# Kernel tuning notes

Measured on AMD Instinct MI355X. Metric: run time of the kernel, lower is better.

The kernel has to match this reference:

```python
import jax, jax.numpy as jnp
import numpy as np

M, N, K = 1024, 11008, 4096


def _unpack_i2u(Bp):
    """Unpack 2-bit unsigned weights per decode_i2u_to_i8s interleave.

    Bp: [N, K//4] int8 storage. Within each group of 4 bytes (16 elements),
    output element at position 4*i + j = (byte_j >> (2*i)) & 3.
    Returns [N, K] int8 with values in {0,1,2,3}.
    """
    Bu = jax.lax.bitcast_convert_type(Bp, jnp.uint8)  # [N, K//4]
    n, kc = Bu.shape
    Bg = Bu.reshape(n, kc // 4, 1, 4)                 # [N, G, 1, j]
    shifts = (jnp.arange(4, dtype=jnp.uint8) * jnp.uint8(2)).reshape(1, 1, 4, 1)
    vals = (Bg >> shifts) & jnp.uint8(3)              # [N, G, i, j]
    return vals.reshape(n, kc * 4).astype(jnp.int8)   # [N, K]


def setup_inputs() -> dict:
    key = jax.random.key(0)
    k1, k2 = jax.random.split(key)
    A = jax.random.randint(k1, (M, K), -128, 128, dtype=jnp.int8)
    B = jax.random.randint(k2, (N, K // 4), -128, 128, dtype=jnp.int8)
    return {"A": A, "B": B}


def reference(A, B):
    W = _unpack_i2u(B)  # [N, K] int8
    C = jax.lax.dot_general(
        A, W,
        dimension_numbers=(((1,), (1,)), ((), ())),
        preferred_element_type=jnp.int32,
    )  # [M, N] int32
    return C
```

## Files before the change

### kernel.cpp

```cpp
#include <hip/hip_runtime.h>
#include <stdint.h>


#define MM 1024
#define NN 11008
#define KK 4096
#define KSTEPS 64
#define MTILES 8
#define NTILES 86
#define NBLOCKS (MTILES * NTILES)
#define STRIDE_A ((size_t)MTILES * 8192)
#define STRIDE_B ((size_t)NTILES * 2048)

using i32x4  = __attribute__((ext_vector_type(4))) int;
using i32x16 = __attribute__((ext_vector_type(16))) int;

__device__ __forceinline__ int pack4(i32x4 v) {
    return (int)(((uint32_t)v[0] & 0xFFu) | (((uint32_t)v[1] & 0xFFu) << 8)
               | (((uint32_t)v[2] & 0xFFu) << 16) | (((uint32_t)v[3] & 0xFFu) << 24));
}

__global__ __launch_bounds__(256) void prep_AB(const int* __restrict__ Asrc,
                                               const int* __restrict__ Bsrc,
                                               uint8_t* __restrict__ A2,
                                               uint8_t* __restrict__ B3) {
    if (blockIdx.x < 1024) {
        const int g = blockIdx.x * 256 + threadIdx.x;
        const int kstep = g >> 12;
        const int rem   = g & 4095;
        const int mtile = rem >> 9;
        const int c     = rem & 511;
        const int row32 = (c >> 7) & 3, kk2 = (c >> 6) & 1;
        const int lane  = c & 63;
        const int row   = mtile * 128 + row32 * 32 + (lane & 31);
        const int kbyte = kstep * 64 + kk2 * 32 + (lane >> 5) * 16;
        const i32x4* s4 = (const i32x4*)(Asrc + (size_t)row * KK + kbyte);
        i32x4 o;
#pragma unroll
        for (int q = 0; q < 4; ++q) o[q] = pack4(s4[q]);
        *(i32x4*)(A2 + (size_t)g * 16) = o;
    } else {
        const int t = (blockIdx.x - 1024) * 256 + threadIdx.x;
        const int n = t >> 6, kstep = t & 63;
        const int ntile = n >> 7, wc = (n >> 6) & 1, ni = (n >> 5) & 1, l31 = n & 31;
        const i32x4* s4 = (const i32x4*)(Bsrc + (size_t)n * (KK / 4) + kstep * 16);
        int w[4];
#pragma unroll
        for (int j = 0; j < 4; ++j) w[j] = pack4(s4[j]);
        uint8_t* base = B3 + ((size_t)kstep * NTILES + ntile) * 2048 + wc * 1024;
        *(int2*)(base + l31 * 16 + ni * 8)        = make_int2(w[0], w[2]);
        *(int2*)(base + (l31 + 32) * 16 + ni * 8) = make_int2(w[1], w[3]);
    }
}

#define GLOAD_LDS16(g, l) __builtin_amdgcn_global_load_lds(                    \
        (const __attribute__((address_space(1))) uint32_t*)(g),                \
        (__attribute__((address_space(3))) uint32_t*)(l), 16, 0, 0)

#define MFMA_I8 __builtin_amdgcn_mfma_i32_32x32x32_i8

#define STAGE(KS, SLOT) do {                                                   \
    const uint8_t* at_ = gA + (size_t)(KS) * STRIDE_A;                         \
    GLOAD_LDS16(at_,        &As[SLOT][wave * 1024]);                           \
    GLOAD_LDS16(at_ + 4096, &As[SLOT][4096 + wave * 1024]);                    \
} while (0)

#define BLOAD(BI, KS) bb[BI] = *(const i32x4*)(gB + (size_t)(KS) * STRIDE_B)

#define COMP(SLOT, BI) do {                                                    \
    _Pragma("unroll")                                                          \
    for (int kk2_ = 0; kk2_ < 2; ++kk2_) {                                     \
        i32x4 a0_ = *(const i32x4*)(&As[SLOT][(wr * 2 + 0) * 2048 + kk2_ * 1024 + lane * 16]); \
        i32x4 a1_ = *(const i32x4*)(&As[SLOT][(wr * 2 + 1) * 2048 + kk2_ * 1024 + lane * 16]); \
        const uint32_t q0_ = (uint32_t)bb[BI][0 * 2 + kk2_];                   \
        const uint32_t q1_ = (uint32_t)bb[BI][1 * 2 + kk2_];                   \
        i32x4 b0_, b1_;                                                        \
        _Pragma("unroll")                                                      \
        for (int i_ = 0; i_ < 4; ++i_) {                                       \
            b0_[i_] = (int)((q0_ >> (2 * i_)) & 0x03030303u);                  \
            b1_[i_] = (int)((q1_ >> (2 * i_)) & 0x03030303u);                  \
        }                                                                      \
        acc[0][0] = MFMA_I8(a0_, b0_, acc[0][0], 0, 0, 0);                     \
        acc[0][1] = MFMA_I8(a0_, b1_, acc[0][1], 0, 0, 0);                     \
        acc[1][0] = MFMA_I8(a1_, b0_, acc[1][0], 0, 0, 0);                     \
        acc[1][1] = MFMA_I8(a1_, b1_, acc[1][1], 0, 0, 0);                     \
    }                                                                          \
} while (0)

#define ITER(T, SLOT, BCUR, BNXT, NW, DOSTAGE, DOB) do {                       \
    asm volatile("s_waitcnt vmcnt(" #NW ")" ::: "memory");                     \
    __builtin_amdgcn_s_barrier();                                              \
    asm volatile("" ::: "memory");                                             \
    __builtin_amdgcn_sched_barrier(0);                                         \
    if (DOSTAGE) STAGE((T) + 5, ((SLOT) + 5) % 6);                             \
    if (DOB) BLOAD(BNXT, (T) + 2);                                             \
    COMP(SLOT, BCUR);                                                          \
} while (0)

__global__ __launch_bounds__(256, 3) void bitnet_gemm(const uint8_t* __restrict__ A2,
                                                      const uint8_t* __restrict__ B3,
                                                      int* __restrict__ C) {
    const int tid  = threadIdx.x;
    const int lane = tid & 63, wave = tid >> 6;
    const int wr   = wave >> 1, wc = wave & 1;
    const int l31  = lane & 31, h = lane >> 5;

    const int bid = blockIdx.x;
    const int l   = (bid & 7) * (NBLOCKS / 8) + (bid >> 3);
    const int bm  = l & 7;
    const int bn  = l >> 3;

    __shared__ __align__(16) uint8_t As[6][8192];

    const uint8_t* gA = A2 + (size_t)bm * 8192 + tid * 16;
    const uint8_t* gB = B3 + (size_t)bn * 2048 + wc * 1024 + lane * 16;

    i32x16 acc[2][2] = {};
    i32x4 bb[3];

    STAGE(0, 0); STAGE(1, 1); STAGE(2, 2); STAGE(3, 3); STAGE(4, 4);
    BLOAD(0, 0); BLOAD(1, 1);

#pragma unroll 1
    for (int t = 0; t < 54; t += 6) {
        ITER(t + 0, 0, 0, 2, 10, true, true);
        ITER(t + 1, 1, 1, 0, 10, true, true);
        ITER(t + 2, 2, 2, 1, 10, true, true);
        ITER(t + 3, 3, 0, 2, 10, true, true);
        ITER(t + 4, 4, 1, 0, 10, true, true);
        ITER(t + 5, 5, 2, 1, 10, true, true);
    }
    ITER(54, 0, 0, 2, 10, true,  true);
    ITER(55, 1, 1, 0, 10, true,  true);
    ITER(56, 2, 2, 1, 10, true,  true);
    ITER(57, 3, 0, 2, 10, true,  true);
    ITER(58, 4, 1, 0, 10, true,  true);
    ITER(59, 5, 2, 1, 10, false, true);
    ITER(60, 0, 0, 2, 10, false, true);
    ITER(61, 1, 1, 0, 8,  false, true);
    ITER(62, 2, 2, 1, 6,  false, false);
    ITER(63, 3, 0, 2, 4,  false, false);

    const int brow = bm * 128, bcol = bn * 128;
#pragma unroll
    for (int mi = 0; mi < 2; ++mi)
#pragma unroll
        for (int ni = 0; ni < 2; ++ni) {
            const int colg = bcol + wc * 64 + ni * 32 + l31;
#pragma unroll
            for (int r = 0; r < 16; ++r) {
                const int rowin = (r & 3) + 8 * (r >> 2) + 4 * h;
                const int rowg  = brow + wr * 64 + mi * 32 + rowin;
                C[(size_t)rowg * NN + colg] = acc[mi][ni][r];
            }
        }
}

extern "C" void kernel_launch(void* const* d_in, const int* in_sizes, int n_in,
                              void* d_out, int out_size, void* d_ws, size_t ws_size,
                              hipStream_t stream) {
    const int* A32 = (const int*)d_in[0];
    const int* B32 = (const int*)d_in[1];
    int* C = (int*)d_out;

    uint8_t* A2 = (uint8_t*)d_ws;
    uint8_t* B3 = A2 + (size_t)MM * KK;

    prep_AB<<<dim3(1024 + 2752), dim3(256), 0, stream>>>(A32, B32, A2, B3);
    bitnet_gemm<<<dim3(NBLOCKS), dim3(256), 0, stream>>>(A2, B3, C);
}
```

Before: 64.43 us.

## Process two k-steps per barrier with triple-buffered 16KB LDS stages

Restructures the main loop so each iteration consumes two 64-wide k-steps. Each stage is a 16KB LDS buffer, triple-buffered instead of the previous six 8KB slots, and B register prefetch is reduced to one double-k-step ahead. This halves the number of barriers and waitcnt points per K loop and issues larger batches of async loads. The cost is a shallower prefetch depth in k-steps, which may expose more global memory latency.

```diff
diff --git a/kernel.cpp b/kernel.cpp
--- a/kernel.cpp
+++ b/kernel.cpp
@@ -5,7 +5,6 @@
 #define MM 1024
 #define NN 11008
 #define KK 4096
-#define KSTEPS 64
 #define MTILES 8
 #define NTILES 86
 #define NBLOCKS (MTILES * NTILES)
@@ -42,12 +41,12 @@
     } else {
         const int t = (blockIdx.x - 1024) * 256 + threadIdx.x;
         const int n = t >> 6, kstep = t & 63;
-        const int ntile = n >> 7, wc = (n >> 6) & 1, ni = (n >> 5) & 1, l31 = n & 31;
+        const int ntile = n >> 7, hf = (n >> 6) & 1, ni = (n >> 5) & 1, l31 = n & 31;
         const i32x4* s4 = (const i32x4*)(Bsrc + (size_t)n * (KK / 4) + kstep * 16);
         int w[4];
 #pragma unroll
         for (int j = 0; j < 4; ++j) w[j] = pack4(s4[j]);
-        uint8_t* base = B3 + ((size_t)kstep * NTILES + ntile) * 2048 + wc * 1024;
+        uint8_t* base = B3 + ((size_t)kstep * NTILES + ntile) * 2048 + hf * 1024;
         *(int2*)(base + l31 * 16 + ni * 8)        = make_int2(w[0], w[2]);
         *(int2*)(base + (l31 + 32) * 16 + ni * 8) = make_int2(w[1], w[3]);
     }
@@ -59,42 +58,57 @@
 
 #define MFMA_I8 __builtin_amdgcn_mfma_i32_32x32x32_i8
 
-#define STAGE(KS, SLOT) do {                                                   \
-    const uint8_t* at_ = gA + (size_t)(KS) * STRIDE_A;                         \
-    GLOAD_LDS16(at_,        &As[SLOT][wave * 1024]);                           \
-    GLOAD_LDS16(at_ + 4096, &As[SLOT][4096 + wave * 1024]);                    \
+#define STAGE2(SL, T2) do {                                                    \
+    const uint8_t* s0_ = gA + (size_t)(2 * (T2)) * STRIDE_A;                   \
+    const uint8_t* s1_ = s0_ + STRIDE_A;                                       \
+    uint8_t* l_ = &As[SL][0];                                                  \
+    GLOAD_LDS16(s0_,        l_ + wave * 1024);                                 \
+    GLOAD_LDS16(s0_ + 4096, l_ + 4096 + wave * 1024);                          \
+    GLOAD_LDS16(s1_,        l_ + 8192 + wave * 1024);                          \
+    GLOAD_LDS16(s1_ + 4096, l_ + 12288 + wave * 1024);                         \
 } while (0)
 
-#define BLOAD(BI, KS) bb[BI] = *(const i32x4*)(gB + (size_t)(KS) * STRIDE_B)
+#define BLOAD2(BI, T2) do {                                                    \
+    bb0[BI] = *(const i32x4*)(gB + (size_t)(2 * (T2)) * STRIDE_B);             \
+    bb1[BI] = *(const i32x4*)(gB + (size_t)(2 * (T2) + 1) * STRIDE_B);         \
+} while (0)
 
-#define COMP(SLOT, BI) do {                                                    \
+#define COMP2(SL, BI) do {                                                     \
     _Pragma("unroll")                                                          \
-    for (int kk2_ = 0; kk2_ < 2; ++kk2_) {                                     \
-        i32x4 a0_ = *(const i32x4*)(&As[SLOT][(wr * 2 + 0) * 2048 + kk2_ * 1024 + lane * 16]); \
-        i32x4 a1_ = *(const i32x4*)(&As[SLOT][(wr * 2 + 1) * 2048 + kk2_ * 1024 + lane * 16]); \
-        const uint32_t q0_ = (uint32_t)bb[BI][0 * 2 + kk2_];                   \
-        const uint32_t q1_ = (uint32_t)bb[BI][1 * 2 + kk2_];                   \
-        i32x4 b0_, b1_;                                                        \
+    for (int sub_ = 0; sub_ < 2; ++sub_) {                                     \
+        const uint8_t* ab_ = &As[SL][sub_ * 8192];                             \
+        const i32x4 bv_ = sub_ ? bb1[BI] : bb0[BI];                            \
+        i32x4 aA0_ = *(const i32x4*)(ab_ + (wr * 2 + 0) * 2048 + lane * 16);   \
+        i32x4 aA1_ = *(const i32x4*)(ab_ + (wr * 2 + 0) * 2048 + 1024 + lane * 16); \
+        i32x4 aB0_ = *(const i32x4*)(ab_ + (wr * 2 + 1) * 2048 + lane * 16);   \
+        i32x4 aB1_ = *(const i32x4*)(ab_ + (wr * 2 + 1) * 2048 + 1024 + lane * 16); \
         _Pragma("unroll")                                                      \
-        for (int i_ = 0; i_ < 4; ++i_) {                                       \
-            b0_[i_] = (int)((q0_ >> (2 * i_)) & 0x03030303u);                  \
-            b1_[i_] = (int)((q1_ >> (2 * i_)) & 0x03030303u);                  \
+        for (int kk2_ = 0; kk2_ < 2; ++kk2_) {                                 \
+            const uint32_t q0_ = (uint32_t)bv_[kk2_];                          \
+            const uint32_t q1_ = (uint32_t)bv_[2 + kk2_];                      \
+            i32x4 b0_, b1_;                                                    \
+            _Pragma("unroll")                                                  \
+            for (int i_ = 0; i_ < 4; ++i_) {                                   \
+                b0_[i_] = (int)((q0_ >> (2 * i_)) & 0x03030303u);              \
+                b1_[i_] = (int)((q1_ >> (2 * i_)) & 0x03030303u);              \
+            }                                                                  \
+            const i32x4 am0_ = kk2_ ? aA1_ : aA0_;                             \
+            const i32x4 am1_ = kk2_ ? aB1_ : aB0_;                             \
+            acc[0][0] = MFMA_I8(am0_, b0_, acc[0][0], 0, 0, 0);                \
+            acc[0][1] = MFMA_I8(am0_, b1_, acc[0][1], 0, 0, 0);                \
+            acc[1][0] = MFMA_I8(am1_, b0_, acc[1][0], 0, 0, 0);                \
+            acc[1][1] = MFMA_I8(am1_, b1_, acc[1][1], 0, 0, 0);                \
         }                                                                      \
-        acc[0][0] = MFMA_I8(a0_, b0_, acc[0][0], 0, 0, 0);                     \
-        acc[0][1] = MFMA_I8(a0_, b1_, acc[0][1], 0, 0, 0);                     \
-        acc[1][0] = MFMA_I8(a1_, b0_, acc[1][0], 0, 0, 0);                     \
-        acc[1][1] = MFMA_I8(a1_, b1_, acc[1][1], 0, 0, 0);                     \
     }                                                                          \
 } while (0)
 
-#define ITER(T, SLOT, BCUR, BNXT, NW, DOSTAGE, DOB) do {                       \
+#define ITER2(T, SL, SLN, BI, BN, NW, DS, DB) do {                             \
     asm volatile("s_waitcnt vmcnt(" #NW ")" ::: "memory");                     \
     __builtin_amdgcn_s_barrier();                                              \
-    asm volatile("" ::: "memory");                                             \
     __builtin_amdgcn_sched_barrier(0);                                         \
-    if (DOSTAGE) STAGE((T) + 5, ((SLOT) + 5) % 6);                             \
-    if (DOB) BLOAD(BNXT, (T) + 2);                                             \
-    COMP(SLOT, BCUR);                                                          \
+    if (DB) BLOAD2(BN, (T) + 1);                                               \
+    if (DS) STAGE2(SLN, (T) + 2);                                              \
+    COMP2(SL, BI);                                                             \
 } while (0)
 
 __global__ __launch_bounds__(256, 3) void bitnet_gemm(const uint8_t* __restrict__ A2,
@@ -110,36 +124,29 @@
     const int bm  = l & 7;
     const int bn  = l >> 3;
 
-    __shared__ __align__(16) uint8_t As[6][8192];
+    __shared__ __align__(16) uint8_t As[3][16384];
 
     const uint8_t* gA = A2 + (size_t)bm * 8192 + tid * 16;
     const uint8_t* gB = B3 + (size_t)bn * 2048 + wc * 1024 + lane * 16;
 
     i32x16 acc[2][2] = {};
-    i32x4 bb[3];
+    i32x4 bb0[2], bb1[2];
 
-    STAGE(0, 0); STAGE(1, 1); STAGE(2, 2); STAGE(3, 3); STAGE(4, 4);
-    BLOAD(0, 0); BLOAD(1, 1);
+    BLOAD2(0, 0);
+    STAGE2(0, 0);
+    STAGE2(1, 1);
 
 #pragma unroll 1
-    for (int t = 0; t < 54; t += 6) {
-        ITER(t + 0, 0, 0, 2, 10, true, true);
-        ITER(t + 1, 1, 1, 0, 10, true, true);
-        ITER(t + 2, 2, 2, 1, 10, true, true);
-        ITER(t + 3, 3, 0, 2, 10, true, true);
-        ITER(t + 4, 4, 1, 0, 10, true, true);
-        ITER(t + 5, 5, 2, 1, 10, true, true);
+    for (int t = 0; t < 30; t += 6) {
+        ITER2(t + 0, 0, 2, 0, 1, 4, 1, 1);
+        ITER2(t + 1, 1, 0, 1, 0, 4, 1, 1);
+        ITER2(t + 2, 2, 1, 0, 1, 4, 1, 1);
+        ITER2(t + 3, 0, 2, 1, 0, 4, 1, 1);
+        ITER2(t + 4, 1, 0, 0, 1, 4, 1, 1);
+        ITER2(t + 5, 2, 1, 1, 0, 4, 1, 1);
     }
-    ITER(54, 0, 0, 2, 10, true,  true);
-    ITER(55, 1, 1, 0, 10, true,  true);
-    ITER(56, 2, 2, 1, 10, true,  true);
-    ITER(57, 3, 0, 2, 10, true,  true);
-    ITER(58, 4, 1, 0, 10, true,  true);
-    ITER(59, 5, 2, 1, 10, false, true);
-    ITER(60, 0, 0, 2, 10, false, true);
-    ITER(61, 1, 1, 0, 8,  false, true);
-    ITER(62, 2, 2, 1, 6,  false, false);
-    ITER(63, 3, 0, 2, 4,  false, false);
+    ITER2(30, 0, 2, 0, 1, 4, 0, 1);
+    ITER2(31, 1, 0, 1, 0, 0, 0, 0);
 
     const int brow = bm * 128, bcol = bn * 128;
 #pragma unroll
```

Result: slower. 66.02 us (+2.5%).

## Stage B weights through LDS alongside A in a four-slot pipeline

Applied to the files above, without the earlier changes.

Packed B weights now go to LDS through global_load_lds, issued by waves 0-1 alongside the A tile, replacing the per-wave register loads of B. The LDS ring drops from six A-only slots of 8192 bytes to four slots of 10240 bytes (A plus B), so prefetch depth falls from five stages to three. Per-wave vmcnt waits differ because only two waves issue the extra B load. This removes duplicate global B reads between the two row-waves and frees VGPRs, at the cost of shallower prefetch and an extra LDS read per step.

```diff
diff --git a/kernel.cpp b/kernel.cpp
--- a/kernel.cpp
+++ b/kernel.cpp
@@ -5,7 +5,6 @@
 #define MM 1024
 #define NN 11008
 #define KK 4096
-#define KSTEPS 64
 #define MTILES 8
 #define NTILES 86
 #define NBLOCKS (MTILES * NTILES)
@@ -42,12 +41,12 @@
     } else {
         const int t = (blockIdx.x - 1024) * 256 + threadIdx.x;
         const int n = t >> 6, kstep = t & 63;
-        const int ntile = n >> 7, wc = (n >> 6) & 1, ni = (n >> 5) & 1, l31 = n & 31;
+        const int ntile = n >> 7, hf = (n >> 6) & 1, ni = (n >> 5) & 1, l31 = n & 31;
         const i32x4* s4 = (const i32x4*)(Bsrc + (size_t)n * (KK / 4) + kstep * 16);
         int w[4];
 #pragma unroll
         for (int j = 0; j < 4; ++j) w[j] = pack4(s4[j]);
-        uint8_t* base = B3 + ((size_t)kstep * NTILES + ntile) * 2048 + wc * 1024;
+        uint8_t* base = B3 + ((size_t)kstep * NTILES + ntile) * 2048 + hf * 1024;
         *(int2*)(base + l31 * 16 + ni * 8)        = make_int2(w[0], w[2]);
         *(int2*)(base + (l31 + 32) * 16 + ni * 8) = make_int2(w[1], w[3]);
     }
@@ -59,42 +58,52 @@
 
 #define MFMA_I8 __builtin_amdgcn_mfma_i32_32x32x32_i8
 
-#define STAGE(KS, SLOT) do {                                                   \
-    const uint8_t* at_ = gA + (size_t)(KS) * STRIDE_A;                         \
-    GLOAD_LDS16(at_,        &As[SLOT][wave * 1024]);                           \
-    GLOAD_LDS16(at_ + 4096, &As[SLOT][4096 + wave * 1024]);                    \
+#define STAGE(SL, T) do {                                                      \
+    const uint8_t* at_ = gA + (size_t)(T) * STRIDE_A;                          \
+    uint8_t* l_ = &As[SL][0];                                                  \
+    GLOAD_LDS16(at_,        l_ + wave * 1024);                                 \
+    GLOAD_LDS16(at_ + 4096, l_ + 4096 + wave * 1024);                          \
+    if (wave < 2)                                                              \
+        GLOAD_LDS16(gBs + (size_t)(T) * STRIDE_B, l_ + 8192 + wave * 1024);    \
 } while (0)
 
-#define BLOAD(BI, KS) bb[BI] = *(const i32x4*)(gB + (size_t)(KS) * STRIDE_B)
-
-#define COMP(SLOT, BI) do {                                                    \
+#define COMP(SL) do {                                                          \
+    const uint8_t* ab_ = &As[SL][0];                                           \
+    i32x4 aA0_ = *(const i32x4*)(ab_ + (wr * 2 + 0) * 2048 + lane * 16);       \
+    i32x4 aA1_ = *(const i32x4*)(ab_ + (wr * 2 + 0) * 2048 + 1024 + lane * 16);\
+    i32x4 aB0_ = *(const i32x4*)(ab_ + (wr * 2 + 1) * 2048 + lane * 16);       \
+    i32x4 aB1_ = *(const i32x4*)(ab_ + (wr * 2 + 1) * 2048 + 1024 + lane * 16);\
+    const i32x4 bv_ = *(const i32x4*)(ab_ + 8192 + wc * 1024 + lane * 16);     \
     _Pragma("unroll")                                                          \
     for (int kk2_ = 0; kk2_ < 2; ++kk2_) {                                     \
-        i32x4 a0_ = *(const i32x4*)(&As[SLOT][(wr * 2 + 0) * 2048 + kk2_ * 1024 + lane * 16]); \
-        i32x4 a1_ = *(const i32x4*)(&As[SLOT][(wr * 2 + 1) * 2048 + kk2_ * 1024 + lane * 16]); \
-        const uint32_t q0_ = (uint32_t)bb[BI][0 * 2 + kk2_];                   \
-        const uint32_t q1_ = (uint32_t)bb[BI][1 * 2 + kk2_];                   \
+        const uint32_t q0_ = (uint32_t)bv_[kk2_];                              \
+        const uint32_t q1_ = (uint32_t)bv_[2 + kk2_];                          \
         i32x4 b0_, b1_;                                                        \
         _Pragma("unroll")                                                      \
         for (int i_ = 0; i_ < 4; ++i_) {                                       \
             b0_[i_] = (int)((q0_ >> (2 * i_)) & 0x03030303u);                  \
             b1_[i_] = (int)((q1_ >> (2 * i_)) & 0x03030303u);                  \
         }                                                                      \
-        acc[0][0] = MFMA_I8(a0_, b0_, acc[0][0], 0, 0, 0);                     \
-        acc[0][1] = MFMA_I8(a0_, b1_, acc[0][1], 0, 0, 0);                     \
-        acc[1][0] = MFMA_I8(a1_, b0_, acc[1][0], 0, 0, 0);                     \
-        acc[1][1] = MFMA_I8(a1_, b1_, acc[1][1], 0, 0, 0);                     \
+        const i32x4 am0_ = kk2_ ? aA1_ : aA0_;                                 \
+        const i32x4 am1_ = kk2_ ? aB1_ : aB0_;                                 \
+        acc[0][0] = MFMA_I8(am0_, b0_, acc[0][0], 0, 0, 0);                    \
+        acc[0][1] = MFMA_I8(am0_, b1_, acc[0][1], 0, 0, 0);                    \
+        acc[1][0] = MFMA_I8(am1_, b0_, acc[1][0], 0, 0, 0);                    \
+        acc[1][1] = MFMA_I8(am1_, b1_, acc[1][1], 0, 0, 0);                    \
     }                                                                          \
 } while (0)
 
-#define ITER(T, SLOT, BCUR, BNXT, NW, DOSTAGE, DOB) do {                       \
-    asm volatile("s_waitcnt vmcnt(" #NW ")" ::: "memory");                     \
+#define WAITN(N0, N2) do {                                                     \
+    if (wave < 2) asm volatile("s_waitcnt vmcnt(" #N0 ")" ::: "memory");       \
+    else          asm volatile("s_waitcnt vmcnt(" #N2 ")" ::: "memory");       \
+} while (0)
+
+#define ITER(T, NW0, NW2, DS) do {                                             \
+    WAITN(NW0, NW2);                                                           \
     __builtin_amdgcn_s_barrier();                                              \
-    asm volatile("" ::: "memory");                                             \
     __builtin_amdgcn_sched_barrier(0);                                         \
-    if (DOSTAGE) STAGE((T) + 5, ((SLOT) + 5) % 6);                             \
-    if (DOB) BLOAD(BNXT, (T) + 2);                                             \
-    COMP(SLOT, BCUR);                                                          \
+    if (DS) STAGE(((T) + 3) & 3, (T) + 3);                                     \
+    COMP((T) & 3);                                                             \
 } while (0)
 
 __global__ __launch_bounds__(256, 3) void bitnet_gemm(const uint8_t* __restrict__ A2,
@@ -110,36 +119,28 @@
     const int bm  = l & 7;
     const int bn  = l >> 3;
 
-    __shared__ __align__(16) uint8_t As[6][8192];
+    __shared__ __align__(16) uint8_t As[4][10240];
 
-    const uint8_t* gA = A2 + (size_t)bm * 8192 + tid * 16;
-    const uint8_t* gB = B3 + (size_t)bn * 2048 + wc * 1024 + lane * 16;
+    const uint8_t* gA  = A2 + (size_t)bm * 8192 + tid * 16;
+    const uint8_t* gBs = B3 + (size_t)bn * 2048 + wave * 1024 + lane * 16;
 
     i32x16 acc[2][2] = {};
-    i32x4 bb[3];
 
-    STAGE(0, 0); STAGE(1, 1); STAGE(2, 2); STAGE(3, 3); STAGE(4, 4);
-    BLOAD(0, 0); BLOAD(1, 1);
+    STAGE(0, 0);
+    STAGE(1, 1);
+    STAGE(2, 2);
 
 #pragma unroll 1
-    for (int t = 0; t < 54; t += 6) {
-        ITER(t + 0, 0, 0, 2, 10, true, true);
-        ITER(t + 1, 1, 1, 0, 10, true, true);
-        ITER(t + 2, 2, 2, 1, 10, true, true);
-        ITER(t + 3, 3, 0, 2, 10, true, true);
-        ITER(t + 4, 4, 1, 0, 10, true, true);
-        ITER(t + 5, 5, 2, 1, 10, true, true);
+    for (int t = 0; t < 60; t += 4) {
+        ITER(t + 0, 6, 4, 1);
+        ITER(t + 1, 6, 4, 1);
+        ITER(t + 2, 6, 4, 1);
+        ITER(t + 3, 6, 4, 1);
     }
-    ITER(54, 0, 0, 2, 10, true,  true);
-    ITER(55, 1, 1, 0, 10, true,  true);
-    ITER(56, 2, 2, 1, 10, true,  true);
-    ITER(57, 3, 0, 2, 10, true,  true);
-    ITER(58, 4, 1, 0, 10, true,  true);
-    ITER(59, 5, 2, 1, 10, false, true);
-    ITER(60, 0, 0, 2, 10, false, true);
-    ITER(61, 1, 1, 0, 8,  false, true);
-    ITER(62, 2, 2, 1, 6,  false, false);
-    ITER(63, 3, 0, 2, 4,  false, false);
+    ITER(60, 6, 4, 1);
+    ITER(61, 6, 4, 0);
+    ITER(62, 3, 2, 0);
+    ITER(63, 0, 0, 0);
 
     const int brow = bm * 128, bcol = bn * 128;
 #pragma unroll
```

Result: slower. 65.97 us (+2.4%).
